# Optimization experiments

Measured on AMD Instinct MI355X. Metric: run time of the kernel, lower is better.

The kernel has to match this reference:

```python
import jax, jax.numpy as jnp
import numpy as np

D_MODEL = 512
D_FF = 2048
D_K = 64
N_HEADS = 8
LN_EPS = 1e-5


def layer_norm(x, gamma, beta):
    mu = jnp.mean(x, axis=-1, keepdims=True)
    var = jnp.mean(jnp.square(x - mu), axis=-1, keepdims=True)
    return (x - mu) * jax.lax.rsqrt(var + LN_EPS) * gamma + beta


def setup_inputs() -> dict:
    key = jax.random.key(0)
    ks = jax.random.split(key, 8)
    B, S = 16, 1024
    s_in = 1.0 / np.sqrt(D_MODEL)
    s_ff = 1.0 / np.sqrt(D_FF)
    return {
        "x": jax.random.normal(ks[0], (B, S, D_MODEL), jnp.float32),
        # shared QKV projection (the module uses ONE linear for Q, K and V)
        "w_qkv": jax.random.uniform(ks[1], (D_MODEL, D_MODEL), jnp.float32, -s_in, s_in),
        "b_qkv": jnp.zeros((D_MODEL,), jnp.float32),
        "w_out": jax.random.uniform(ks[2], (D_MODEL, D_MODEL), jnp.float32, -s_in, s_in),
        "b_out": jnp.zeros((D_MODEL,), jnp.float32),
        "w1": jax.random.uniform(ks[3], (D_FF, D_MODEL), jnp.float32, -s_in, s_in),
        "b1": jnp.zeros((D_FF,), jnp.float32),
        "w2": jax.random.uniform(ks[4], (D_MODEL, D_FF), jnp.float32, -s_ff, s_ff),
        "b2": jnp.zeros((D_MODEL,), jnp.float32),
        "g1": jnp.ones((D_MODEL,), jnp.float32),
        "be1": jnp.zeros((D_MODEL,), jnp.float32),
        "g2": jnp.ones((D_MODEL,), jnp.float32),
        "be2": jnp.zeros((D_MODEL,), jnp.float32),
    }


def reference(x, w_qkv, b_qkv, w_out, b_out, w1, b1, w2, b2, g1, be1, g2, be2):
    B, S, _ = x.shape
    # --- MultiHeadAttention (shared linear for Q/K/V, dropout = identity) ---
    qkv = x @ w_qkv.T + b_qkv                       # [B,S,D]
    h = qkv.reshape(B, S, N_HEADS, D_K)             # Q = K = V
    scores = jnp.einsum("bqhd,bkhd->bhqk", h, h) / np.sqrt(D_K)
    probs = jax.nn.softmax(scores, axis=-1)
    ctx = jnp.einsum("bhqk,bkhd->bqhd", probs, h).reshape(B, S, D_MODEL)
    attn = ctx @ w_out.T + b_out
    # --- dual-LayerNorm residual #1: x = norm1(x) + norm1(attn) ---
    x = layer_norm(x, g1, be1) + layer_norm(attn, g1, be1)
    # --- FFN ---
    ffn = jax.nn.relu(x @ w1.T + b1) @ w2.T + b2
    # --- residual #2: x = x + norm2(ffn) ---
    return x + layer_norm(ffn, g2, be2)
```

## Files before the change

kernel.cpp:

```cpp
#include <hip/hip_runtime.h>
#include <hip/hip_bf16.h>
#include <stdint.h>


using bf16 = __bf16;
typedef __attribute__((ext_vector_type(2))) __bf16 bf16x2;
typedef __attribute__((ext_vector_type(4))) __bf16 bf16x4;
typedef __attribute__((ext_vector_type(8))) __bf16 bf16x8;
typedef __attribute__((ext_vector_type(4))) float floatx4;
typedef __attribute__((ext_vector_type(16))) float f32x16;

#define AS1 __attribute__((address_space(1)))
#define AS3 __attribute__((address_space(3)))

#define L2E 1.44269504088896340736f

constexpr int BN_ = 16, SQ_ = 1024, DM_ = 512, DFF_ = 2048, NH_ = 8, DK_ = 64;
constexpr int ROWS_ = BN_ * SQ_;

__global__ __launch_bounds__(256) void f2b_kernel(const float* __restrict__ in,
                                                  bf16* __restrict__ out, int n8) {
  int i = blockIdx.x * 256 + threadIdx.x;
  if (i >= n8) return;
  float4 a = ((const float4*)in)[2 * i];
  float4 b = ((const float4*)in)[2 * i + 1];
  bf16x8 o;
  o[0] = (bf16)a.x; o[1] = (bf16)a.y; o[2] = (bf16)a.z; o[3] = (bf16)a.w;
  o[4] = (bf16)b.x; o[5] = (bf16)b.y; o[6] = (bf16)b.z; o[7] = (bf16)b.w;
  ((bf16x8*)out)[i] = o;
}

template <int RELU>
__global__ __launch_bounds__(256) void gemm_bt(const bf16* __restrict__ A,
                                               const bf16* __restrict__ B,
                                               const float* __restrict__ bias,
                                               bf16* __restrict__ C,
                                               int M, int N, int K) {
  __shared__ char glds[32768];
  const int tid = threadIdx.x;
  const int lane = tid & 63;
  const int wv = tid >> 6;
  const int wr = wv >> 1, wc = wv & 1;
  const int r15 = lane & 15, g = lane >> 4;
  const int tileN = blockIdx.x * 128;
  const int tileM = blockIdx.y * 128;

  floatx4 acc[4][4] = {};

  uint32_t dstoff[2];
  const bf16* srcA[2];
  const bf16* srcB[2];
#pragma unroll
  for (int is = 0; is < 2; ++is) {
    const int base = wv * 2048 + is * 1024;
    const int ob = base + lane * 16;
    const int row = ob >> 6;
    const int pslot = (ob >> 4) & 3;
    const int sslot = pslot ^ ((row >> 1) & 3);
    dstoff[is] = base;
    srcA[is] = A + (size_t)(tileM + row) * K + sslot * 8;
    srcB[is] = B + (size_t)(tileN + row) * K + sslot * 8;
  }

#define GSTAGE(buf, kt)                                                         \
  {                                                                             \
    _Pragma("unroll")                                                           \
    for (int is = 0; is < 2; ++is) {                                            \
      __builtin_amdgcn_global_load_lds(                                         \
          (AS1 uint32_t*)(srcA[is] + (kt) * 32),                                \
          (AS3 uint32_t*)((AS3 char*)glds + (buf) * 8192 + dstoff[is]), 16, 0, 0); \
      __builtin_amdgcn_global_load_lds(                                         \
          (AS1 uint32_t*)(srcB[is] + (kt) * 32),                                \
          (AS3 uint32_t*)((AS3 char*)glds + 16384 + (buf) * 8192 + dstoff[is]), \
          16, 0, 0);                                                            \
    }                                                                           \
  }

  uint32_t aoff[4], boff[4];
#pragma unroll
  for (int m = 0; m < 4; ++m) {
    const int arow = wr * 64 + m * 16 + r15;
    aoff[m] = (uint32_t)((arow * 64 + g * 16) ^ (((arow >> 1) & 3) << 4));
  }
#pragma unroll
  for (int n = 0; n < 4; ++n) {
    const int brow = wc * 64 + n * 16 + r15;
    boff[n] = (uint32_t)((brow * 64 + g * 16) ^ (((brow >> 1) & 3) << 4));
  }

  const int nk = K >> 5;
  GSTAGE(0, 0);

  for (int kt = 0; kt < nk; ++kt) {
    const int cur = kt & 1;
    if (kt + 1 < nk) {
      GSTAGE(cur ^ 1, kt + 1);
      asm volatile("s_waitcnt vmcnt(4)" ::: "memory");
    } else {
      asm volatile("s_waitcnt vmcnt(0)" ::: "memory");
    }
    __builtin_amdgcn_s_barrier();
    __builtin_amdgcn_sched_barrier(0);

    const char* Ac = (const char*)glds + cur * 8192;
    const char* Bc = (const char*)glds + 16384 + cur * 8192;

    bf16x8 af[4], bfr[4];
#pragma unroll
    for (int m = 0; m < 4; ++m) af[m] = *(const bf16x8*)(Ac + aoff[m]);
#pragma unroll
    for (int n = 0; n < 4; ++n) bfr[n] = *(const bf16x8*)(Bc + boff[n]);
#pragma unroll
    for (int m = 0; m < 4; ++m)
#pragma unroll
      for (int n = 0; n < 4; ++n)
        acc[m][n] = __builtin_amdgcn_mfma_f32_16x16x32_bf16(af[m], bfr[n],
                                                            acc[m][n], 0, 0, 0);
    __builtin_amdgcn_s_barrier();
  }
#undef GSTAGE

#pragma unroll
  for (int n = 0; n < 4; ++n) {
    const int col = tileN + wc * 64 + n * 16 + r15;
    const float bv = bias[col];
#pragma unroll
    for (int m = 0; m < 4; ++m) {
      const int row0 = tileM + wr * 64 + m * 16 + g * 4;
#pragma unroll
      for (int j = 0; j < 4; ++j) {
        float v = acc[m][n][j] + bv;
        if (RELU) v = fmaxf(v, 0.f);
        C[(size_t)(row0 + j) * N + col] = (bf16)v;
      }
    }
  }
}

__global__ __launch_bounds__(256) void attn_kernel(const bf16* __restrict__ qkv,
                                                   bf16* __restrict__ ctx) {
  __shared__ char lds[16384];

  const int tid = threadIdx.x;
  const int lane = tid & 63;
  const int wv = tid >> 6;
  const int l31 = lane & 31;
  const int h = lane >> 5;
  const int b = blockIdx.z, hd = blockIdx.y, qt = blockIdx.x;
  const size_t headoff = (size_t)b * SQ_ * DM_ + hd * DK_;
  const int q0 = qt * 128 + wv * 32;

  const float QS = 0.125f * L2E;
  bf16x8 aq[4];
#pragma unroll
  for (int kd = 0; kd < 4; ++kd) {
    const bf16* gq = qkv + headoff + (size_t)(q0 + l31) * DM_ + kd * 16 + h * 8;
    bf16x8 v = *(const bf16x8*)gq;
#pragma unroll
    for (int e = 0; e < 8; ++e) v[e] = (bf16)((float)v[e] * QS);
    aq[kd] = v;
  }

  f32x16 o0 = {}, o1 = {};
  float mstate = -1e30f, lstate = 0.f;

  const uint32_t ldsb = (uint32_t)(uintptr_t)(AS3 char*)lds;

  uint32_t dstoff[2];
  const bf16* srcb[2];
#pragma unroll
  for (int is = 0; is < 2; ++is) {
    const int ob = is * 4096 + wv * 1024 + lane * 16;
    const int e0 = ob >> 1;
    const int srow = ((e0 >> 8) << 2) + ((e0 >> 4) & 3);
    const int dcol = ((e0 >> 6) & 3) * 16 + ((e0 >> 3) & 1) * 8;
    dstoff[is] = is * 4096 + wv * 1024;
    srcb[is] = qkv + headoff + (size_t)srow * DM_ + dcol;
  }

#define STAGE(buf, t)                                                          \
  {                                                                            \
    _Pragma("unroll")                                                          \
    for (int is = 0; is < 2; ++is) {                                           \
      __builtin_amdgcn_global_load_lds(                                        \
          (AS1 uint32_t*)(srcb[is] + (size_t)(t) * 64 * DM_),                  \
          (AS3 uint32_t*)((AS3 char*)lds + (buf) * 8192 + dstoff[is]), 16, 0, 0); \
    }                                                                          \
  }

  constexpr int NT = SQ_ / 64;
  STAGE(0, 0);

  for (int t = 0; t < NT; ++t) {
    const int cur = t & 1;
    __builtin_amdgcn_s_barrier();
    if (t + 1 < NT) {
      STAGE(cur ^ 1, t + 1);
      asm volatile("s_waitcnt vmcnt(2)" ::: "memory");
    } else {
      asm volatile("s_waitcnt vmcnt(0)" ::: "memory");
    }
    __builtin_amdgcn_s_barrier();
    __builtin_amdgcn_sched_barrier(0);

    const char* tile = (const char*)lds + cur * 8192;

    f32x16 s0v = {}, s1v = {};
    const char* pabase = tile + (l31 >> 2) * 512 + (l31 & 3) * 32 + h * 16;
    __builtin_amdgcn_s_setprio(1);
#pragma unroll
    for (int kd = 0; kd < 4; ++kd) {
      bf16x8 a0 = *(const bf16x8*)(pabase + kd * 128);
      bf16x8 a1 = *(const bf16x8*)(pabase + kd * 128 + 4096);
      s0v = __builtin_amdgcn_mfma_f32_32x32x16_bf16(a0, aq[kd], s0v, 0, 0, 0);
      s1v = __builtin_amdgcn_mfma_f32_32x32x16_bf16(a1, aq[kd], s1v, 0, 0, 0);
    }
    __builtin_amdgcn_s_setprio(0);

    float mx = s0v[0];
#pragma unroll
    for (int r = 1; r < 16; ++r) mx = fmaxf(mx, s0v[r]);
#pragma unroll
    for (int r = 0; r < 16; ++r) mx = fmaxf(mx, s1v[r]);
    mx = fmaxf(mx, __shfl_xor(mx, 32));
    if (!__all(mx - mstate <= 8.f)) {
      const float nm = fmaxf(mstate, mx);
      const float al = exp2f(mstate - nm);
      mstate = nm;
      lstate *= al;
#pragma unroll
      for (int r = 0; r < 16; ++r) { o0[r] *= al; o1[r] *= al; }
    }
    float rs = 0.f;
#pragma unroll
    for (int r = 0; r < 16; ++r) {
      float p = exp2f(s0v[r] - mstate);
      s0v[r] = p; rs += p;
    }
#pragma unroll
    for (int r = 0; r < 16; ++r) {
      float p = exp2f(s1v[r] - mstate);
      s1v[r] = p; rs += p;
    }
    rs += __shfl_xor(rs, 32);
    lstate += rs;

    uint32_t pf[4][4];
#pragma unroll
    for (int ks = 0; ks < 4; ++ks) {
      const int kb = (ks & 1) * 8;
      float v0, v1, v2, v3, v4, v5, v6, v7;
      if (ks < 2) {
        v0 = s0v[kb+0]; v1 = s0v[kb+1]; v2 = s0v[kb+2]; v3 = s0v[kb+3];
        v4 = s0v[kb+4]; v5 = s0v[kb+5]; v6 = s0v[kb+6]; v7 = s0v[kb+7];
      } else {
        v0 = s1v[kb+0]; v1 = s1v[kb+1]; v2 = s1v[kb+2]; v3 = s1v[kb+3];
        v4 = s1v[kb+4]; v5 = s1v[kb+5]; v6 = s1v[kb+6]; v7 = s1v[kb+7];
      }
      union { bf16x2 v; uint32_t u; } P0, P1, P2, P3;
      P0.v = bf16x2{(bf16)v0, (bf16)v1};
      P1.v = bf16x2{(bf16)v2, (bf16)v3};
      P2.v = bf16x2{(bf16)v4, (bf16)v5};
      P3.v = bf16x2{(bf16)v6, (bf16)v7};
      asm volatile("v_permlane32_swap_b32 %0, %1" : "+v"(P0.u), "+v"(P2.u));
      asm volatile("v_permlane32_swap_b32 %0, %1" : "+v"(P1.u), "+v"(P3.u));
      pf[ks][0] = P0.u;
      pf[ks][1] = P1.u;
      pf[ks][2] = P2.u;
      pf[ks][3] = P3.u;
    }

#pragma unroll
    for (int df = 0; df < 2; ++df) {
      const uint32_t vb = ldsb + cur * 8192 + df * 256 + (lane & 15) * 8 +
                          ((lane >> 4) & 1) * 128 + (lane >> 5) * 1024;
      bf16x4 lo[4], hi[4];
#pragma unroll
      for (int ks = 0; ks < 4; ++ks) {
        asm volatile("ds_read_b64_tr_b16 %0, %2\n\t"
                     "ds_read_b64_tr_b16 %1, %2 offset:512"
                     : "=&v"(lo[ks]), "=&v"(hi[ks])
                     : "v"(vb + ks * 2048));
      }
      asm volatile("s_waitcnt lgkmcnt(0)" ::: "memory");
      __builtin_amdgcn_sched_barrier(0);
      __builtin_amdgcn_s_setprio(1);
#pragma unroll
      for (int ks = 0; ks < 4; ++ks) {
        union { struct { bf16x4 l, h; } p; bf16x8 v; } av;
        av.p.l = lo[ks]; av.p.h = hi[ks];
        union { uint32_t u[4]; bf16x8 v; } bv;
        bv.u[0] = pf[ks][0]; bv.u[1] = pf[ks][1];
        bv.u[2] = pf[ks][2]; bv.u[3] = pf[ks][3];
        if (df == 0)
          o0 = __builtin_amdgcn_mfma_f32_32x32x16_bf16(av.v, bv.v, o0, 0, 0, 0);
        else
          o1 = __builtin_amdgcn_mfma_f32_32x32x16_bf16(av.v, bv.v, o1, 0, 0, 0);
      }
      __builtin_amdgcn_s_setprio(0);
    }
  }
#undef STAGE

  __syncthreads();
  const float invl = 1.f / lstate;
  char* wb = (char*)lds + wv * 4096;
#pragma unroll
  for (int df = 0; df < 2; ++df)
#pragma unroll
    for (int t = 0; t < 4; ++t) {
      const f32x16& ov = df ? o1 : o0;
      bf16x4 pkt;
      pkt[0] = (bf16)(ov[4*t+0] * invl);
      pkt[1] = (bf16)(ov[4*t+1] * invl);
      pkt[2] = (bf16)(ov[4*t+2] * invl);
      pkt[3] = (bf16)(ov[4*t+3] * invl);
      const int byte = (l31 * 128 + df * 64 + t * 16 + h * 8) ^ ((l31 & 7) << 4);
      *(bf16x4*)(wb + byte) = pkt;
    }
#pragma unroll
  for (int ps = 0; ps < 4; ++ps) {
    const int qr = ps * 8 + (lane >> 3);
    const int byte = (qr * 128 + (lane & 7) * 16) ^ ((qr & 7) << 4);
    bf16x8 vv = *(const bf16x8*)(wb + byte);
    bf16* dst = ctx + (size_t)(b * SQ_ + q0 + qr) * DM_ + hd * 64 + (lane & 7) * 8;
    *(bf16x8*)dst = vv;
  }
}

__global__ __launch_bounds__(256) void dual_ln_kernel(const float* __restrict__ x,
                                                      const bf16* __restrict__ attn,
                                                      const float* __restrict__ g1,
                                                      const float* __restrict__ be1,
                                                      bf16* __restrict__ out) {
  const int row = blockIdx.x * 4 + (threadIdx.x >> 6);
  const int lane = threadIdx.x & 63;
  const float* xr = x + (size_t)row * DM_ + lane * 8;
  float xs[8], as_[8];
  float4 t0 = ((const float4*)xr)[0];
  float4 t1 = ((const float4*)xr)[1];
  xs[0] = t0.x; xs[1] = t0.y; xs[2] = t0.z; xs[3] = t0.w;
  xs[4] = t1.x; xs[5] = t1.y; xs[6] = t1.z; xs[7] = t1.w;
  bf16x8 av = *(const bf16x8*)(attn + (size_t)row * DM_ + lane * 8);
#pragma unroll
  for (int e = 0; e < 8; ++e) as_[e] = (float)av[e];
  float sx = 0, sx2 = 0, sa = 0, sa2 = 0;
#pragma unroll
  for (int e = 0; e < 8; ++e) {
    sx += xs[e]; sx2 += xs[e] * xs[e];
    sa += as_[e]; sa2 += as_[e] * as_[e];
  }
#pragma unroll
  for (int off = 1; off < 64; off <<= 1) {
    sx += __shfl_xor(sx, off);  sx2 += __shfl_xor(sx2, off);
    sa += __shfl_xor(sa, off);  sa2 += __shfl_xor(sa2, off);
  }
  const float inv = 1.f / (float)DM_;
  const float mux = sx * inv, mua = sa * inv;
  const float rx = rsqrtf(fmaxf(sx2 * inv - mux * mux, 0.f) + 1e-5f);
  const float ra = rsqrtf(fmaxf(sa2 * inv - mua * mua, 0.f) + 1e-5f);
  bf16x8 ov;
#pragma unroll
  for (int e = 0; e < 8; ++e) {
    const int c = lane * 8 + e;
    const float val = ((xs[e] - mux) * rx + (as_[e] - mua) * ra) * g1[c] + 2.f * be1[c];
    ov[e] = (bf16)val;
  }
  *(bf16x8*)(out + (size_t)row * DM_ + lane * 8) = ov;
}

__global__ __launch_bounds__(256) void final_ln_kernel(const bf16* __restrict__ x1,
                                                       const bf16* __restrict__ ffn,
                                                       const float* __restrict__ g2,
                                                       const float* __restrict__ be2,
                                                       float* __restrict__ out) {
  const int row = blockIdx.x * 4 + (threadIdx.x >> 6);
  const int lane = threadIdx.x & 63;
  bf16x8 xv = *(const bf16x8*)(x1 + (size_t)row * DM_ + lane * 8);
  bf16x8 fv = *(const bf16x8*)(ffn + (size_t)row * DM_ + lane * 8);
  float fs[8];
#pragma unroll
  for (int e = 0; e < 8; ++e) fs[e] = (float)fv[e];
  float sf = 0, sf2 = 0;
#pragma unroll
  for (int e = 0; e < 8; ++e) { sf += fs[e]; sf2 += fs[e] * fs[e]; }
#pragma unroll
  for (int off = 1; off < 64; off <<= 1) {
    sf += __shfl_xor(sf, off);  sf2 += __shfl_xor(sf2, off);
  }
  const float inv = 1.f / (float)DM_;
  const float mu = sf * inv;
  const float rs = rsqrtf(fmaxf(sf2 * inv - mu * mu, 0.f) + 1e-5f);
  float ov[8];
#pragma unroll
  for (int e = 0; e < 8; ++e) {
    const int c = lane * 8 + e;
    ov[e] = (float)xv[e] + (fs[e] - mu) * rs * g2[c] + be2[c];
  }
  float* orow = out + (size_t)row * DM_ + lane * 8;
  float4 o0 = {ov[0], ov[1], ov[2], ov[3]};
  float4 o1 = {ov[4], ov[5], ov[6], ov[7]};
  ((float4*)orow)[0] = o0;
  ((float4*)orow)[1] = o1;
}

extern "C" void kernel_launch(void* const* d_in, const int* in_sizes, int n_in,
                              void* d_out, int out_size, void* d_ws, size_t ws_size,
                              hipStream_t stream) {
  const float* x     = (const float*)d_in[0];
  const float* w_qkv = (const float*)d_in[1];
  const float* b_qkv = (const float*)d_in[2];
  const float* w_out = (const float*)d_in[3];
  const float* b_out = (const float*)d_in[4];
  const float* w1    = (const float*)d_in[5];
  const float* b1    = (const float*)d_in[6];
  const float* w2    = (const float*)d_in[7];
  const float* b2    = (const float*)d_in[8];
  const float* g1    = (const float*)d_in[9];
  const float* be1   = (const float*)d_in[10];
  const float* g2    = (const float*)d_in[11];
  const float* be2   = (const float*)d_in[12];
  float* out = (float*)d_out;

  char* ws = (char*)d_ws;
  const size_t o_wqkv = 0;
  const size_t o_wout = o_wqkv + (size_t)DM_ * DM_ * 2;
  const size_t o_w1   = o_wout + (size_t)DM_ * DM_ * 2;
  const size_t o_w2   = o_w1 + (size_t)DFF_ * DM_ * 2;
  const size_t o_A    = o_w2 + (size_t)DM_ * DFF_ * 2;
  const size_t o_B    = o_A + (size_t)ROWS_ * DM_ * 2;
  const size_t o_C    = o_B + (size_t)ROWS_ * DM_ * 2;
  const size_t o_D    = o_C + (size_t)ROWS_ * DM_ * 2;
  const size_t need   = o_D + (size_t)ROWS_ * DFF_ * 2;
  if (ws_size < need) return;

  bf16* wqkv_bf = (bf16*)(ws + o_wqkv);
  bf16* wout_bf = (bf16*)(ws + o_wout);
  bf16* w1_bf   = (bf16*)(ws + o_w1);
  bf16* w2_bf   = (bf16*)(ws + o_w2);
  bf16* bufA    = (bf16*)(ws + o_A);
  bf16* bufB    = (bf16*)(ws + o_B);
  bf16* bufC    = (bf16*)(ws + o_C);
  bf16* bufD    = (bf16*)(ws + o_D);

  f2b_kernel<<<dim3((ROWS_ * DM_ / 8 + 255) / 256), dim3(256), 0, stream>>>(x, bufA, ROWS_ * DM_ / 8);
  f2b_kernel<<<dim3((DM_ * DM_ / 8 + 255) / 256), dim3(256), 0, stream>>>(w_qkv, wqkv_bf, DM_ * DM_ / 8);
  f2b_kernel<<<dim3((DM_ * DM_ / 8 + 255) / 256), dim3(256), 0, stream>>>(w_out, wout_bf, DM_ * DM_ / 8);
  f2b_kernel<<<dim3((DFF_ * DM_ / 8 + 255) / 256), dim3(256), 0, stream>>>(w1, w1_bf, DFF_ * DM_ / 8);
  f2b_kernel<<<dim3((DM_ * DFF_ / 8 + 255) / 256), dim3(256), 0, stream>>>(w2, w2_bf, DM_ * DFF_ / 8);

  gemm_bt<0><<<dim3(DM_ / 128, ROWS_ / 128), dim3(256), 0, stream>>>(bufA, wqkv_bf, b_qkv, bufB, ROWS_, DM_, DM_);

  attn_kernel<<<dim3(SQ_ / 128, NH_, BN_), dim3(256), 0, stream>>>(bufB, bufA);

  gemm_bt<0><<<dim3(DM_ / 128, ROWS_ / 128), dim3(256), 0, stream>>>(bufA, wout_bf, b_out, bufC, ROWS_, DM_, DM_);

  dual_ln_kernel<<<dim3(ROWS_ / 4), dim3(256), 0, stream>>>(x, bufC, g1, be1, bufB);

  gemm_bt<1><<<dim3(DFF_ / 128, ROWS_ / 128), dim3(256), 0, stream>>>(bufB, w1_bf, b1, bufD, ROWS_, DFF_, DM_);

  gemm_bt<0><<<dim3(DM_ / 128, ROWS_ / 128), dim3(256), 0, stream>>>(bufD, w2_bf, b2, bufC, ROWS_, DM_, DFF_);

  final_ln_kernel<<<dim3(ROWS_ / 4), dim3(256), 0, stream>>>(bufB, bufC, g2, be2, out);
}
```

Measured before the change: 238.5 us.

## Merge conversion kernels, tree-reduce softmax stats, read bf16 x in dual LayerNorm

Replaces five float-to-bf16 conversion launches with one kernel that dispatches on flat index, to cut launch overhead. The softmax row max and sum in attention use tree and multi-accumulator reductions to shorten dependency chains. The dual LayerNorm reads the bf16 copy of x kept in a spare buffer instead of the fp32 input, halving that read traffic. The trade is slightly lower precision in the x normalization.

```diff
diff --git a/kernel.cpp b/kernel.cpp
--- a/kernel.cpp
+++ b/kernel.cpp
@@ -18,16 +18,28 @@
 constexpr int BN_ = 16, SQ_ = 1024, DM_ = 512, DFF_ = 2048, NH_ = 8, DK_ = 64;
 constexpr int ROWS_ = BN_ * SQ_;
 
-__global__ __launch_bounds__(256) void f2b_kernel(const float* __restrict__ in,
-                                                  bf16* __restrict__ out, int n8) {
-  int i = blockIdx.x * 256 + threadIdx.x;
-  if (i >= n8) return;
+__device__ __forceinline__ void f2b_one(const float* __restrict__ in,
+                                        bf16* __restrict__ out, int i) {
   float4 a = ((const float4*)in)[2 * i];
   float4 b = ((const float4*)in)[2 * i + 1];
   bf16x8 o;
   o[0] = (bf16)a.x; o[1] = (bf16)a.y; o[2] = (bf16)a.z; o[3] = (bf16)a.w;
   o[4] = (bf16)b.x; o[5] = (bf16)b.y; o[6] = (bf16)b.z; o[7] = (bf16)b.w;
   ((bf16x8*)out)[i] = o;
+}
+
+__global__ __launch_bounds__(256) void f2b5_kernel(
+    const float* __restrict__ s0, bf16* __restrict__ d0, int n0,
+    const float* __restrict__ s1, bf16* __restrict__ d1, int n1,
+    const float* __restrict__ s2, bf16* __restrict__ d2, int n2,
+    const float* __restrict__ s3, bf16* __restrict__ d3, int n3,
+    const float* __restrict__ s4, bf16* __restrict__ d4, int n4) {
+  int i = blockIdx.x * 256 + threadIdx.x;
+  if (i < n0) { f2b_one(s0, d0, i); return; }  i -= n0;
+  if (i < n1) { f2b_one(s1, d1, i); return; }  i -= n1;
+  if (i < n2) { f2b_one(s2, d2, i); return; }  i -= n2;
+  if (i < n3) { f2b_one(s3, d3, i); return; }  i -= n3;
+  if (i < n4) { f2b_one(s4, d4, i); }
 }
 
 template <int RELU>
@@ -217,11 +229,13 @@
     }
     __builtin_amdgcn_s_setprio(0);
 
-    float mx = s0v[0];
-#pragma unroll
-    for (int r = 1; r < 16; ++r) mx = fmaxf(mx, s0v[r]);
-#pragma unroll
-    for (int r = 0; r < 16; ++r) mx = fmaxf(mx, s1v[r]);
+    float t8[8];
+#pragma unroll
+    for (int r = 0; r < 8; ++r)
+      t8[r] = fmaxf(fmaxf(s0v[r], s0v[r + 8]), fmaxf(s1v[r], s1v[r + 8]));
+    float t4a = fmaxf(t8[0], t8[4]), t4b = fmaxf(t8[1], t8[5]);
+    float t4c = fmaxf(t8[2], t8[6]), t4d = fmaxf(t8[3], t8[7]);
+    float mx = fmaxf(fmaxf(t4a, t4b), fmaxf(t4c, t4d));
     mx = fmaxf(mx, __shfl_xor(mx, 32));
     if (!__all(mx - mstate <= 8.f)) {
       const float nm = fmaxf(mstate, mx);
@@ -231,17 +245,22 @@
 #pragma unroll
       for (int r = 0; r < 16; ++r) { o0[r] *= al; o1[r] *= al; }
     }
-    float rs = 0.f;
-#pragma unroll
-    for (int r = 0; r < 16; ++r) {
-      float p = exp2f(s0v[r] - mstate);
-      s0v[r] = p; rs += p;
-    }
-#pragma unroll
-    for (int r = 0; r < 16; ++r) {
-      float p = exp2f(s1v[r] - mstate);
-      s1v[r] = p; rs += p;
-    }
+    float r0 = 0.f, r1 = 0.f, r2 = 0.f, r3 = 0.f;
+#pragma unroll
+    for (int r = 0; r < 16; r += 4) {
+      float p0 = exp2f(s0v[r + 0] - mstate); s0v[r + 0] = p0; r0 += p0;
+      float p1 = exp2f(s0v[r + 1] - mstate); s0v[r + 1] = p1; r1 += p1;
+      float p2 = exp2f(s0v[r + 2] - mstate); s0v[r + 2] = p2; r2 += p2;
+      float p3 = exp2f(s0v[r + 3] - mstate); s0v[r + 3] = p3; r3 += p3;
+    }
+#pragma unroll
+    for (int r = 0; r < 16; r += 4) {
+      float p0 = exp2f(s1v[r + 0] - mstate); s1v[r + 0] = p0; r0 += p0;
+      float p1 = exp2f(s1v[r + 1] - mstate); s1v[r + 1] = p1; r1 += p1;
+      float p2 = exp2f(s1v[r + 2] - mstate); s1v[r + 2] = p2; r2 += p2;
+      float p3 = exp2f(s1v[r + 3] - mstate); s1v[r + 3] = p3; r3 += p3;
+    }
+    float rs = (r0 + r1) + (r2 + r3);
     rs += __shfl_xor(rs, 32);
     lstate += rs;
 
@@ -328,22 +347,18 @@
   }
 }
 
-__global__ __launch_bounds__(256) void dual_ln_kernel(const float* __restrict__ x,
+__global__ __launch_bounds__(256) void dual_ln_kernel(const bf16* __restrict__ x,
                                                       const bf16* __restrict__ attn,
                                                       const float* __restrict__ g1,
                                                       const float* __restrict__ be1,
                                                       bf16* __restrict__ out) {
   const int row = blockIdx.x * 4 + (threadIdx.x >> 6);
   const int lane = threadIdx.x & 63;
-  const float* xr = x + (size_t)row * DM_ + lane * 8;
+  bf16x8 xv = *(const bf16x8*)(x + (size_t)row * DM_ + lane * 8);
+  bf16x8 av = *(const bf16x8*)(attn + (size_t)row * DM_ + lane * 8);
   float xs[8], as_[8];
-  float4 t0 = ((const float4*)xr)[0];
-  float4 t1 = ((const float4*)xr)[1];
-  xs[0] = t0.x; xs[1] = t0.y; xs[2] = t0.z; xs[3] = t0.w;
-  xs[4] = t1.x; xs[5] = t1.y; xs[6] = t1.z; xs[7] = t1.w;
-  bf16x8 av = *(const bf16x8*)(attn + (size_t)row * DM_ + lane * 8);
-#pragma unroll
-  for (int e = 0; e < 8; ++e) as_[e] = (float)av[e];
+#pragma unroll
+  for (int e = 0; e < 8; ++e) { xs[e] = (float)xv[e]; as_[e] = (float)av[e]; }
   float sx = 0, sx2 = 0, sa = 0, sa2 = 0;
 #pragma unroll
   for (int e = 0; e < 8; ++e) {
@@ -443,19 +458,24 @@
   bf16* bufC    = (bf16*)(ws + o_C);
   bf16* bufD    = (bf16*)(ws + o_D);
 
-  f2b_kernel<<<dim3((ROWS_ * DM_ / 8 + 255) / 256), dim3(256), 0, stream>>>(x, bufA, ROWS_ * DM_ / 8);
-  f2b_kernel<<<dim3((DM_ * DM_ / 8 + 255) / 256), dim3(256), 0, stream>>>(w_qkv, wqkv_bf, DM_ * DM_ / 8);
-  f2b_kernel<<<dim3((DM_ * DM_ / 8 + 255) / 256), dim3(256), 0, stream>>>(w_out, wout_bf, DM_ * DM_ / 8);
-  f2b_kernel<<<dim3((DFF_ * DM_ / 8 + 255) / 256), dim3(256), 0, stream>>>(w1, w1_bf, DFF_ * DM_ / 8);
-  f2b_kernel<<<dim3((DM_ * DFF_ / 8 + 255) / 256), dim3(256), 0, stream>>>(w2, w2_bf, DM_ * DFF_ / 8);
-
-  gemm_bt<0><<<dim3(DM_ / 128, ROWS_ / 128), dim3(256), 0, stream>>>(bufA, wqkv_bf, b_qkv, bufB, ROWS_, DM_, DM_);
+  const int nx  = ROWS_ * DM_ / 8;
+  const int nwq = DM_ * DM_ / 8;
+  const int nw1 = DFF_ * DM_ / 8;
+  const int ntot = nx + 2 * nwq + 2 * nw1;
+  f2b5_kernel<<<dim3((ntot + 255) / 256), dim3(256), 0, stream>>>(
+      x, bufD, nx,
+      w_qkv, wqkv_bf, nwq,
+      w_out, wout_bf, nwq,
+      w1, w1_bf, nw1,
+      w2, w2_bf, nw1);
+
+  gemm_bt<0><<<dim3(DM_ / 128, ROWS_ / 128), dim3(256), 0, stream>>>(bufD, wqkv_bf, b_qkv, bufB, ROWS_, DM_, DM_);
 
   attn_kernel<<<dim3(SQ_ / 128, NH_, BN_), dim3(256), 0, stream>>>(bufB, bufA);
 
   gemm_bt<0><<<dim3(DM_ / 128, ROWS_ / 128), dim3(256), 0, stream>>>(bufA, wout_bf, b_out, bufC, ROWS_, DM_, DM_);
 
-  dual_ln_kernel<<<dim3(ROWS_ / 4), dim3(256), 0, stream>>>(x, bufC, g1, be1, bufB);
+  dual_ln_kernel<<<dim3(ROWS_ / 4), dim3(256), 0, stream>>>(bufD, bufC, g1, be1, bufB);
 
   gemm_bt<1><<<dim3(DFF_ / 128, ROWS_ / 128), dim3(256), 0, stream>>>(bufB, w1_bf, b1, bufD, ROWS_, DFF_, DM_);
 
```

Measured after the change: 237.6 us. No clear change (-0.4%).
